# Kernel tuning notes

Measured on AMD Instinct MI355X. Metric: run time of the kernel, lower is better.

The kernel has to match this reference:

```python
import jax, jax.numpy as jnp
import numpy as np

B, T, N, M, G = 4, 16, 256, 128, 8
D, H, FFN, FD = 512, 8, 1024, 256
HD = D // H
SCALE = HD ** -0.5
EPS = 1e-5
NL = 6  # num_layers; layer 0 has no self-attn


def _ln(x, g, b):
    mu = x.mean(-1, keepdims=True)
    var = ((x - mu) ** 2).mean(-1, keepdims=True)
    return (x - mu) * jax.lax.rsqrt(var + EPS) * g + b


def setup_inputs() -> dict:
    key = jax.random.key(0)
    ks = jax.random.split(key, 16)
    w = lambda i, shape: jax.random.normal(ks[i], shape, jnp.float32) * 0.02
    return {
        'current_tokens': jax.random.normal(ks[0], (B, T, N, D), jnp.float32),
        'trajectory_tokens': jax.random.normal(ks[1], (G, M, D), jnp.float32),
        'sa_in_w': w(2, (NL - 1, 3 * D, D)), 'sa_in_b': jnp.zeros((NL - 1, 3 * D), jnp.float32),
        'sa_out_w': w(3, (NL - 1, D, D)), 'sa_out_b': jnp.zeros((NL - 1, D), jnp.float32),
        'n1_g': jnp.ones((NL - 1, D), jnp.float32), 'n1_b': jnp.zeros((NL - 1, D), jnp.float32),
        'ca_qw': w(4, (NL, D, D)), 'ca_qb': jnp.zeros((NL, D), jnp.float32),
        'ca_kw': w(5, (NL, D, D)), 'ca_kb': jnp.zeros((NL, D), jnp.float32),
        'ca_vw': w(6, (NL, D, D)), 'ca_vb': jnp.zeros((NL, D), jnp.float32),
        'ca_ow': w(7, (NL, D, D)), 'ca_ob': jnp.zeros((NL, D), jnp.float32),
        'n2_g': jnp.ones((NL, D), jnp.float32), 'n2_b': jnp.zeros((NL, D), jnp.float32),
        'f_w1': w(8, (NL, FFN, D)), 'f_b1': jnp.zeros((NL, FFN), jnp.float32),
        'f_w2': w(9, (NL, D, FFN)), 'f_b2': jnp.zeros((NL, D), jnp.float32),
        'n3_g': jnp.ones((NL, D), jnp.float32), 'n3_b': jnp.zeros((NL, D), jnp.float32),
        'out_w': w(10, (FD, D)), 'out_b': jnp.zeros((FD,), jnp.float32),
        'on_g': jnp.ones((FD,), jnp.float32), 'on_b': jnp.zeros((FD,), jnp.float32),
    }


def reference(current_tokens, trajectory_tokens, sa_in_w, sa_in_b, sa_out_w, sa_out_b,
              n1_g, n1_b, ca_qw, ca_qb, ca_kw, ca_kb, ca_vw, ca_vb, ca_ow, ca_ob,
              n2_g, n2_b, f_w1, f_b1, f_w2, f_b2, n3_g, n3_b, out_w, out_b, on_g, on_b):
    x = current_tokens
    attn_list = []
    for i in range(NL):
        if i >= 1:  # self-attention over detections within each frame
            j = i - 1
            xf = x.reshape(B * T, N, D)
            qkv = xf @ sa_in_w[j].T + sa_in_b[j]
            q, k, v = jnp.split(qkv, 3, axis=-1)
            q = q.reshape(B * T, N, H, HD)
            k = k.reshape(B * T, N, H, HD)
            v = v.reshape(B * T, N, H, HD)
            s = jnp.einsum('bnhd,bmhd->bhnm', q, k) * SCALE
            a = jax.nn.softmax(s, axis=-1)
            o = jnp.einsum('bhnm,bmhd->bnhd', a, v).reshape(B * T, N, D)
            o = o @ sa_out_w[j].T + sa_out_b[j]
            x = _ln(x + o.reshape(B, T, N, D), n1_g[j], n1_b[j])
        # cross-attention against group-averaged trajectory memory
        Q = (x @ ca_qw[i].T + ca_qb[i]).reshape(B, T, N, H, HD)
        K = (trajectory_tokens @ ca_kw[i].T + ca_kb[i]).reshape(G, M, H, HD).mean(0)  # (M,H,HD)
        V = (trajectory_tokens @ ca_vw[i].T + ca_vb[i]).reshape(G, M, H, HD).mean(0)
        s = jnp.einsum('btnhd,mhd->btnhm', Q, K) * SCALE
        # current_times=None => rel_pe_mask is zeros(T,M): no future mask; rel_pe bias is dead code in source
        a = jax.nn.softmax(s, axis=-1)  # (B,T,N,H,M)
        o = jnp.einsum('btnhm,mhd->btnhd', a, V).reshape(B, T, N, D)
        o = o @ ca_ow[i].T + ca_ob[i]
        x = _ln(x + o, n2_g[i], n2_b[i])
        # FFN
        h = jax.nn.relu(x @ f_w1[i].T + f_b1[i]) @ f_w2[i].T + f_b2[i]
        x = _ln(x + h, n3_g[i], n3_b[i])
        attn_list.append(a.mean(axis=2))  # (B,T,H,M) avg over detections
    out = _ln(x @ out_w.T + out_b, on_g, on_b)
    return out, jnp.stack(attn_list)
```

## Files before the change

kernel.cpp:

```cpp
#include <hip/hip_runtime.h>
#include <cstdint>
#include <cstddef>

#define NLl 6
#define SCALEf 0.125f
#define EPSf 1e-5f
#define Hh 8

typedef __attribute__((ext_vector_type(8))) short short8;
typedef __attribute__((ext_vector_type(4))) float float4_;
typedef __attribute__((ext_vector_type(16))) float f32x16;
typedef __attribute__((ext_vector_type(4))) int int4_;
typedef __attribute__((ext_vector_type(2))) int int2_;

__device__ inline float b2f(ushort u){ union{uint i; float f;} v; v.i = ((uint)u)<<16; return v.f; }
__device__ inline ushort f2b(float f){ union{float f; uint i;} v; v.f=f; uint r = v.i + 0x7fffu + ((v.i>>16)&1u); return (ushort)(r>>16); }
__device__ inline void unpack2(uint w, float& lo, float& hi){
  union{uint i; float f;} a,b; a.i = w<<16; b.i = w & 0xffff0000u; lo=a.f; hi=b.f;
}
__device__ inline float wred(float v){
  #pragma unroll
  for(int m=32;m>=1;m>>=1) v += __shfl_xor(v, m, 64);
  return v;
}
__device__ inline f32x16 zero16(){
  f32x16 z;
  #pragma unroll
  for(int r=0;r<16;r++) z[r]=0.f;
  return z;
}
__device__ inline int xcd_swz(int orig, int nwg){
  int q = nwg >> 3, r = nwg & 7;
  int x = orig & 7, idx = orig >> 3;
  return (x < r ? x*(q+1) : r*(q+1) + (x-r)*q) + idx;
}

struct CvtTab {
  const float* s[10];
  ushort* d[10];
  unsigned st[11];
};
__global__ __launch_bounds__(256) void cvt_all(CvtTab tab){
  unsigned g = blockIdx.x*256 + threadIdx.x;
  if (g >= tab.st[10]) return;
  int i = 0;
  #pragma unroll
  for (int k=0;k<9;k++) if (g >= tab.st[k+1]) i = k+1;
  unsigned off = g - tab.st[i];
  float4_ v = *(const float4_*)(tab.s[i] + (size_t)off*4);
  ushort o[4] = {f2b(v[0]),f2b(v[1]),f2b(v[2]),f2b(v[3])};
  *(int2_*)(tab.d[i] + (size_t)off*4) = *(const int2_*)o;
}

__global__ __launch_bounds__(256) void tmean_k(const float* __restrict__ traj, ushort* __restrict__ tm){
  int idx = blockIdx.x*256 + threadIdx.x;
  float s = 0.f;
  #pragma unroll
  for(int g=0; g<8; g++) s += traj[g*65536 + idx];
  tm[idx] = f2b(s*0.125f);
}

template<int RELU, int RESID>
__device__ __forceinline__ void gemm_core(
    const ushort* __restrict__ A, const ushort* __restrict__ W,
    const float* __restrict__ bias, const ushort* __restrict__ R,
    ushort* __restrict__ C,
    int Ndim, int K, int rowA0, int colB0,
    ushort* As, ushort* Bs)
{
  const int tid = threadIdx.x;
  const int wid = tid>>6, lane = tid&63;
  const int wr = wid>>1, wc = wid&1;
  const int l15 = lane & 15, l4 = lane >> 4;

  const ushort* gA[2]; const ushort* gB[2];
  int ldsOff[2];
  #pragma unroll
  for (int s=0;s<2;s++){
    int p = wid*128 + s*64 + lane;
    int lrow = p>>3, x = p&7;
    int logical = x ^ (lrow&7);
    int row = (logical>>2)*64 + lrow;
    int ls = logical&3;
    gA[s] = A + (size_t)(rowA0+row)*K + ls*8;
    gB[s] = W + (size_t)(colB0+row)*K + ls*8;
    ldsOff[s] = wid*1024 + s*512;
  }

  float4_ acc[4][4];
  #pragma unroll
  for(int i=0;i<4;i++)
    #pragma unroll
    for(int j=0;j<4;j++){ acc[i][j][0]=0.f; acc[i][j][1]=0.f; acc[i][j][2]=0.f; acc[i][j][3]=0.f; }

  const int NT = K >> 5;
  #pragma unroll
  for (int s=0;s<2;s++){
    __builtin_amdgcn_global_load_lds((const unsigned int*)gA[s], (unsigned int*)(As + ldsOff[s]), 16, 0, 0);
    __builtin_amdgcn_global_load_lds((const unsigned int*)gB[s], (unsigned int*)(Bs + ldsOff[s]), 16, 0, 0);
    gA[s] += 32; gB[s] += 32;
  }
  if (NT > 1){
    #pragma unroll
    for (int s=0;s<2;s++){
      __builtin_amdgcn_global_load_lds((const unsigned int*)gA[s], (unsigned int*)(As + 4096 + ldsOff[s]), 16, 0, 0);
      __builtin_amdgcn_global_load_lds((const unsigned int*)gB[s], (unsigned int*)(Bs + 4096 + ldsOff[s]), 16, 0, 0);
      gA[s] += 32; gB[s] += 32;
    }
  }

  int cur = 0;
  for (int t=0; t<NT; ++t){
    if (t+1 < NT) asm volatile("s_waitcnt vmcnt(4)" ::: "memory");
    else          asm volatile("s_waitcnt vmcnt(0)" ::: "memory");
    __builtin_amdgcn_s_barrier();
    if (t+2 < NT){
      int nb = cur+2; if (nb>=3) nb-=3;
      #pragma unroll
      for (int s=0;s<2;s++){
        __builtin_amdgcn_global_load_lds((const unsigned int*)gA[s], (unsigned int*)(As + nb*4096 + ldsOff[s]), 16, 0, 0);
        __builtin_amdgcn_global_load_lds((const unsigned int*)gB[s], (unsigned int*)(Bs + nb*4096 + ldsOff[s]), 16, 0, 0);
        gA[s] += 32; gB[s] += 32;
      }
    }
    const ushort* Apt = As + cur*4096;
    const ushort* Bpt = Bs + cur*4096;
    short8 fa[4], fb[4];
    #pragma unroll
    for(int m=0;m<4;m++){
      int lrow = m*16 + l15;
      fa[m] = *(const short8*)&Apt[lrow*64 + (((wr*4 + l4) ^ (l15&7))*8)];
    }
    #pragma unroll
    for(int n=0;n<4;n++){
      int lrow = n*16 + l15;
      fb[n] = *(const short8*)&Bpt[lrow*64 + (((wc*4 + l4) ^ (l15&7))*8)];
    }
    #pragma unroll
    for(int m=0;m<4;m++)
      #pragma unroll
      for(int n=0;n<4;n++)
        acc[m][n] = __builtin_amdgcn_mfma_f32_16x16x32_bf16(fa[m], fb[n], acc[m][n], 0,0,0);
    cur = (cur==2) ? 0 : cur+1;
  }

  #pragma unroll
  for(int m=0;m<4;m++){
    int grow = rowA0 + wr*64 + m*16 + l4*4;
    #pragma unroll
    for(int n=0;n<4;n++){
      int gcol = colB0 + wc*64 + n*16 + l15;
      float bv = bias[gcol];
      #pragma unroll
      for(int r=0;r<4;r++){
        float v = acc[m][n][r] + bv;
        if (RESID) v += b2f(R[(size_t)(grow + r)*512 + gcol]);
        if (RELU) v = fmaxf(v, 0.f);
        C[(size_t)(grow + r)*Ndim + gcol] = f2b(v);
      }
    }
  }
}

template<int RELU, int RESID>
__global__ __launch_bounds__(256, 3) void gemm_bias(
    const ushort* __restrict__ A, const ushort* __restrict__ W,
    const float* __restrict__ bias, const ushort* __restrict__ R,
    ushort* __restrict__ C, int Ndim, int K, int nbx)
{
  __shared__ ushort As[12288];
  __shared__ ushort Bs[12288];
  const int wg = xcd_swz(blockIdx.x, gridDim.x);
  const int bn = wg % nbx, bm = wg / nbx;
  gemm_core<RELU,RESID>(A, W, bias, R, C, Ndim, K, bm*128, bn*128, As, Bs);
}

__global__ __launch_bounds__(256, 3) void kv_all(
    const ushort* __restrict__ tm,
    const ushort* __restrict__ wk, const ushort* __restrict__ wv,
    const float* __restrict__ bk, const float* __restrict__ bv,
    ushort* __restrict__ KVm)
{
  __shared__ ushort As[12288];
  __shared__ ushort Bs[12288];
  const int i = blockIdx.x >> 3;
  const int r8 = blockIdx.x & 7;
  const int which = r8 >> 2, bn = r8 & 3;
  const ushort* W  = (which ? wv : wk) + (size_t)i*262144;
  const float* bias = (which ? bv : bk) + i*512;
  ushort* C = KVm + (size_t)(i*2 + which)*65536;
  gemm_core<0,0>(tm, W, bias, nullptr, C, 512, 512, 0, bn*128, As, Bs);
}

template<int NKEYS, int WRITE_ATTN, int KPF>
__global__ __launch_bounds__(256) void attn_mfma(
  const ushort* __restrict__ Qb, int qstr,
  const ushort* __restrict__ Kb, int kstr,
  const ushort* __restrict__ Vb, int vstr,
  ushort* __restrict__ Ob,
  float* __restrict__ attn_out)
{
  constexpr int NK2 = NKEYS*2;
  __shared__ __align__(16) ushort KsV[NKEYS*64 + 64*NKEYS];
  __shared__ float psum[4][NKEYS];
  const int f = blockIdx.x, h = blockIdx.y;
  const int tid = threadIdx.x, lane = tid & 63, w = tid >> 6;
  const int l31 = lane & 31, l5 = lane >> 5;
  const int swz = (lane & 7) << 4;

  ushort* Ks = KsV;
  ushort* Vt = KsV + NKEYS*64;
  const ushort* kp0 = Kb + (size_t)(KPF ? f*256 : 0)*kstr + h*64;
  const ushort* vp0 = Vb + (size_t)(KPF ? f*256 : 0)*vstr + h*64;

  for (int c = tid; c < NKEYS*8; c += 256){
    int m = c>>3, dc = c&7;
    short8 k8 = *(const short8*)(kp0 + (size_t)m*kstr + dc*8);
    short8 v8 = *(const short8*)(vp0 + (size_t)m*vstr + dc*8);
    *(short8*)((char*)Ks + m*128 + ((dc*16) ^ ((m&7)<<4))) = k8;
    #pragma unroll
    for (int j=0;j<8;j++){
      int d = dc*8 + j;
      *(ushort*)((char*)Vt + d*NK2 + ((m*2) ^ (j<<4))) = (ushort)v8[j];
    }
  }

  short8 qb[2][4];
  const int q0 = w*64;
  const ushort* qp0 = Qb + (size_t)(f*256)*qstr + h*64;
  #pragma unroll
  for (int qj=0;qj<2;qj++)
    #pragma unroll
    for (int dc=0;dc<4;dc++)
      qb[qj][dc] = *(const short8*)(qp0 + (size_t)(q0 + qj*32 + l31)*qstr + dc*16 + l5*8);
  __syncthreads();

  f32x16 O[2][2];
  O[0][0]=zero16(); O[0][1]=zero16(); O[1][0]=zero16(); O[1][1]=zero16();
  float lpart[2] = {0.f, 0.f};

  for (int t = 0; t < NKEYS/32; t++){
    const int k0 = t*32;
    short8 ka[4];
    #pragma unroll
    for (int dc=0;dc<4;dc++)
      ka[dc] = *(const short8*)((char*)Ks + (k0+l31)*128 + (((dc*32) + (l5*16)) ^ swz));
    f32x16 s0 = zero16(), s1 = zero16();
    #pragma unroll
    for (int dc=0;dc<4;dc++){
      s0 = __builtin_amdgcn_mfma_f32_32x32x16_bf16(ka[dc], qb[0][dc], s0, 0,0,0);
      s1 = __builtin_amdgcn_mfma_f32_32x32x16_bf16(ka[dc], qb[1][dc], s1, 0,0,0);
    }
    uint pw[2][8];
    #pragma unroll
    for (int qj=0;qj<2;qj++){
      const f32x16& sv = qj ? s1 : s0;
      float p[16]; float lp = 0.f;
      #pragma unroll
      for (int r=0;r<16;r++){ p[r] = __expf(sv[r]*SCALEf); lp += p[r]; }
      lpart[qj] += lp;
      #pragma unroll
      for (int k=0;k<8;k++){
        uint w_;
        asm("v_cvt_pk_bf16_f32 %0, %1, %2" : "=v"(w_) : "v"(p[2*k]), "v"(p[2*k+1]));
        pw[qj][k] = w_;
      }
    }
    short8 pa[2][2];
    #pragma unroll
    for (int qj=0;qj<2;qj++){
      #pragma unroll
      for (int mj=0;mj<2;mj++){
        uint a0 = pw[qj][mj*4+2], b0 = pw[qj][mj*4+0];
        uint a1 = pw[qj][mj*4+3], b1 = pw[qj][mj*4+1];
        asm("v_permlane32_swap_b32 %0, %1" : "+v"(a0), "+v"(b0));
        asm("v_permlane32_swap_b32 %0, %1" : "+v"(a1), "+v"(b1));
        union { uint u[4]; short8 s8; } u_;
        u_.u[0]=b0; u_.u[1]=b1; u_.u[2]=a0; u_.u[3]=a1;
        pa[qj][mj] = u_.s8;
      }
    }
    #pragma unroll
    for (int mj=0;mj<2;mj++){
      short8 vbf[2];
      #pragma unroll
      for (int dj=0;dj<2;dj++)
        vbf[dj] = *(const short8*)((char*)Vt + (dj*32+l31)*NK2 + (((k0 + mj*16 + l5*8)*2) ^ swz));
      #pragma unroll
      for (int qj=0;qj<2;qj++)
        #pragma unroll
        for (int dj=0;dj<2;dj++)
          O[qj][dj] = __builtin_amdgcn_mfma_f32_32x32x16_bf16(pa[qj][mj], vbf[dj], O[qj][dj], 0,0,0);
    }
  }

  float invl[2];
  #pragma unroll
  for (int qj=0;qj<2;qj++){
    float lt = lpart[qj] + __shfl_xor(lpart[qj], 32, 64);
    invl[qj] = 1.f / lt;
  }

  ushort* op0 = Ob + (size_t)(f*256)*512 + h*64;
  #pragma unroll
  for (int qj=0;qj<2;qj++){
    #pragma unroll
    for (int r=0;r<16;r++){
      int qr = (r&3) + 8*(r>>2) + 4*l5;
      float il = __shfl(invl[qj], (lane & 32) | qr, 64);
      #pragma unroll
      for (int dj=0;dj<2;dj++){
        float v = O[qj][dj][r] * il;
        op0[(size_t)(q0 + qj*32 + qr)*512 + dj*32 + l31] = f2b(v);
      }
    }
  }

  if (WRITE_ATTN){
    for (int t = 0; t < NKEYS/32; t++){
      const int k0 = t*32;
      short8 ka[4];
      #pragma unroll
      for (int dc=0;dc<4;dc++)
        ka[dc] = *(const short8*)((char*)Ks + (k0+l31)*128 + (((dc*32) + (l5*16)) ^ swz));
      f32x16 s0 = zero16(), s1 = zero16();
      #pragma unroll
      for (int dc=0;dc<4;dc++){
        s0 = __builtin_amdgcn_mfma_f32_32x32x16_bf16(ka[dc], qb[0][dc], s0, 0,0,0);
        s1 = __builtin_amdgcn_mfma_f32_32x32x16_bf16(ka[dc], qb[1][dc], s1, 0,0,0);
      }
      float tsum[16];
      #pragma unroll
      for (int r=0;r<16;r++){
        float v = __expf(s0[r]*SCALEf)*invl[0] + __expf(s1[r]*SCALEf)*invl[1];
        #pragma unroll
        for (int mk=1; mk<=16; mk<<=1) v += __shfl_xor(v, mk, 64);
        tsum[r] = v;
      }
      if (l31 == 0){
        #pragma unroll
        for (int r=0;r<16;r++)
          psum[w][k0 + (r&3) + 8*(r>>2) + 4*l5] = tsum[r];
      }
    }
    __syncthreads();
    for (int m = tid; m < NKEYS; m += 256){
      attn_out[f*(Hh*NKEYS) + h*NKEYS + m] =
        (psum[0][m]+psum[1][m]+psum[2][m]+psum[3][m]) * (1.0f/256.0f);
    }
  }
}

__global__ __launch_bounds__(256) void ln_post(
  const ushort* __restrict__ S,
  const float* __restrict__ g, const float* __restrict__ b,
  ushort* __restrict__ Y)
{
  const int row = blockIdx.x*4 + (threadIdx.x>>6);
  const int lane = threadIdx.x & 63;
  uint xw[4];
  *(int4_*)xw = *(const int4_*)(S + (size_t)row*512 + lane*8);
  float v[8];
  #pragma unroll
  for(int j=0;j<4;j++){ unpack2(xw[j], v[2*j], v[2*j+1]); }
  float s=0.f, sq=0.f;
  #pragma unroll
  for(int j=0;j<8;j++){ s += v[j]; sq += v[j]*v[j]; }
  s = wred(s); sq = wred(sq);
  float mu = s * (1.0f/512.0f);
  float var = sq * (1.0f/512.0f) - mu*mu;
  float rs = rsqrtf(var + EPSf);
  ushort ob[8];
  #pragma unroll
  for(int j=0;j<8;j++){
    ob[j] = f2b((v[j]-mu)*rs*g[lane*8+j] + b[lane*8+j]);
  }
  *(int4_*)(Y + (size_t)row*512 + lane*8) = *(const int4_*)ob;
}

__global__ __launch_bounds__(256) void ln_out(
  const ushort* __restrict__ A, const float* __restrict__ g,
  const float* __restrict__ b, float* __restrict__ out)
{
  const int row = blockIdx.x*4 + (threadIdx.x>>6);
  const int lane = threadIdx.x & 63;
  uint aw[2];
  *(int2_*)aw = *(const int2_*)(A + (size_t)row*256 + lane*4);
  float v[4];
  unpack2(aw[0], v[0], v[1]); unpack2(aw[1], v[2], v[3]);
  float s=0.f, sq=0.f;
  #pragma unroll
  for(int j=0;j<4;j++){ s += v[j]; sq += v[j]*v[j]; }
  s = wred(s); sq = wred(sq);
  float mu = s * (1.0f/256.0f);
  float var = sq * (1.0f/256.0f) - mu*mu;
  float rs = rsqrtf(var + EPSf);
  float4_ o;
  #pragma unroll
  for(int j=0;j<4;j++){
    o[j] = (v[j]-mu)*rs*g[lane*4+j] + b[lane*4+j];
  }
  *(float4_*)(out + (size_t)row*256 + lane*4) = o;
}

extern "C" void kernel_launch(void* const* d_in, const int* in_sizes, int n_in,
                              void* d_out, int out_size, void* d_ws, size_t ws_size,
                              hipStream_t stream) {
  const float* cur      = (const float*)d_in[0];
  const float* traj     = (const float*)d_in[1];
  const float* sa_in_w  = (const float*)d_in[2];
  const float* sa_in_b  = (const float*)d_in[3];
  const float* sa_out_w = (const float*)d_in[4];
  const float* sa_out_b = (const float*)d_in[5];
  const float* n1_g     = (const float*)d_in[6];
  const float* n1_b     = (const float*)d_in[7];
  const float* ca_qw    = (const float*)d_in[8];
  const float* ca_qb    = (const float*)d_in[9];
  const float* ca_kw    = (const float*)d_in[10];
  const float* ca_kb    = (const float*)d_in[11];
  const float* ca_vw    = (const float*)d_in[12];
  const float* ca_vb    = (const float*)d_in[13];
  const float* ca_ow    = (const float*)d_in[14];
  const float* ca_ob    = (const float*)d_in[15];
  const float* n2_g     = (const float*)d_in[16];
  const float* n2_b     = (const float*)d_in[17];
  const float* f_w1     = (const float*)d_in[18];
  const float* f_b1     = (const float*)d_in[19];
  const float* f_w2     = (const float*)d_in[20];
  const float* f_b2     = (const float*)d_in[21];
  const float* n3_g     = (const float*)d_in[22];
  const float* n3_b     = (const float*)d_in[23];
  const float* out_w    = (const float*)d_in[24];
  const float* out_b    = (const float*)d_in[25];
  const float* on_g     = (const float*)d_in[26];
  const float* on_b     = (const float*)d_in[27];

  float* out      = (float*)d_out;
  float* attn_out = out + (size_t)4*16*256*256;

  uint8_t* ws = (uint8_t*)d_ws;
  size_t off = 0;
  auto alloc = [&](size_t bytes)->uint8_t*{ uint8_t* p = ws + off; off += (bytes + 255) & ~(size_t)255; return p; };
  ushort* X   = (ushort*)alloc(16777216);
  ushort* B1  = (ushort*)alloc(50331648);
  ushort* B2  = (ushort*)alloc(16777216);
  ushort* KVm = (ushort*)alloc((size_t)6*2*65536*2);
  ushort* tm  = (ushort*)alloc(131072);
  ushort* w_sa_in  = (ushort*)alloc((size_t)5*1536*512*2);
  ushort* w_sa_out = (ushort*)alloc((size_t)5*512*512*2);
  ushort* w_ca_q   = (ushort*)alloc((size_t)6*512*512*2);
  ushort* w_ca_k   = (ushort*)alloc((size_t)6*512*512*2);
  ushort* w_ca_v   = (ushort*)alloc((size_t)6*512*512*2);
  ushort* w_ca_o   = (ushort*)alloc((size_t)6*512*512*2);
  ushort* w_f1     = (ushort*)alloc((size_t)6*1024*512*2);
  ushort* w_f2     = (ushort*)alloc((size_t)6*512*1024*2);
  ushort* w_out    = (ushort*)alloc((size_t)256*512*2);

  CvtTab tab;
  const float* srcs[10] = {cur, sa_in_w, sa_out_w, ca_qw, ca_kw, ca_vw, ca_ow, f_w1, f_w2, out_w};
  ushort* dsts[10]      = {X,   w_sa_in, w_sa_out, w_ca_q, w_ca_k, w_ca_v, w_ca_o, w_f1, w_f2, w_out};
  unsigned lens[10] = {16384u*512u, 5u*1536u*512u, 5u*512u*512u, 6u*512u*512u, 6u*512u*512u,
                       6u*512u*512u, 6u*512u*512u, 6u*1024u*512u, 6u*512u*1024u, 256u*512u};
  unsigned acc4 = 0;
  for (int i=0;i<10;i++){ tab.s[i]=srcs[i]; tab.d[i]=dsts[i]; tab.st[i]=acc4; acc4 += lens[i]/4; }
  tab.st[10] = acc4;
  cvt_all<<<(acc4+255)/256,256,0,stream>>>(tab);
  tmean_k<<<256,256,0,stream>>>(traj, tm);
  kv_all<<<48,256,0,stream>>>(tm, w_ca_k, w_ca_v, ca_kb, ca_vb, KVm);

  for (int i=0;i<NLl;i++){
    if (i>=1){
      int j = i-1;
      gemm_bias<0,0><<<12*128,256,0,stream>>>(X, w_sa_in + (size_t)j*1536*512, sa_in_b + j*1536, nullptr, B1, 1536, 512, 12);
      attn_mfma<256,0,1><<<dim3(64,8),256,0,stream>>>(B1, 1536, B1+512, 1536, B1+1024, 1536, B2, nullptr);
      gemm_bias<0,1><<<4*128,256,0,stream>>>(B2, w_sa_out + (size_t)j*262144, sa_out_b + j*512, X, B1, 512, 512, 4);
      ln_post<<<4096,256,0,stream>>>(B1, n1_g + j*512, n1_b + j*512, X);
    }
    gemm_bias<0,0><<<4*128,256,0,stream>>>(X, w_ca_q + (size_t)i*262144, ca_qb + i*512, nullptr, B2, 512, 512, 4);
    attn_mfma<128,1,0><<<dim3(64,8),256,0,stream>>>(B2, 512, KVm + (size_t)i*131072, 512, KVm + (size_t)i*131072 + 65536, 512, B1, attn_out + (size_t)i*65536);
    gemm_bias<0,1><<<4*128,256,0,stream>>>(B1, w_ca_o + (size_t)i*262144, ca_ob + i*512, X, B2, 512, 512, 4);
    ln_post<<<4096,256,0,stream>>>(B2, n2_g + i*512, n2_b + i*512, X);
    gemm_bias<1,0><<<8*128,256,0,stream>>>(X, w_f1 + (size_t)i*524288, f_b1 + i*1024, nullptr, B1, 1024, 512, 8);
    gemm_bias<0,1><<<4*128,256,0,stream>>>(B1, w_f2 + (size_t)i*524288, f_b2 + i*512, X, B2, 512, 1024, 4);
    ln_post<<<4096,256,0,stream>>>(B2, n3_g + i*512, n3_b + i*512, X);
  }
  gemm_bias<0,0><<<2*128,256,0,stream>>>(X, w_out, out_b, nullptr, B2, 256, 512, 2);
  ln_out<<<4096,256,0,stream>>>(B2, on_g, on_b, out);
}
```

Baseline: 1.316 ms.

## Load GEMM weight fragments directly to registers, drop B LDS tile

The GEMM core no longer stages the weight (B) tile through LDS. Each wave loads its B fragments straight from global memory into registers, double-buffered across an unrolled-by-two K loop, with s_setprio raised around the MFMA block. This halves LDS use per block, which could raise occupancy, and removes the B LDS writes and reads. The cost is redundant global/L2 traffic for weights shared across waves and exposed global-load latency. The attention kernel also reuses the V tile LDS region for psum, adding a barrier, to cut shared memory.

New measurement: 1.742 ms. 32.4% more time.

```diff
diff --git a/kernel.cpp b/kernel.cpp
--- a/kernel.cpp
+++ b/kernel.cpp
@@ -66,14 +66,14 @@
     const float* __restrict__ bias, const ushort* __restrict__ R,
     ushort* __restrict__ C,
     int Ndim, int K, int rowA0, int colB0,
-    ushort* As, ushort* Bs)
+    ushort* As)
 {
   const int tid = threadIdx.x;
   const int wid = tid>>6, lane = tid&63;
   const int wr = wid>>1, wc = wid&1;
   const int l15 = lane & 15, l4 = lane >> 4;
 
-  const ushort* gA[2]; const ushort* gB[2];
+  const ushort* gA[2];
   int ldsOff[2];
   #pragma unroll
   for (int s=0;s<2;s++){
@@ -83,9 +83,12 @@
     int row = (logical>>2)*64 + lrow;
     int ls = logical&3;
     gA[s] = A + (size_t)(rowA0+row)*K + ls*8;
-    gB[s] = W + (size_t)(colB0+row)*K + ls*8;
     ldsOff[s] = wid*1024 + s*512;
   }
+  const ushort* wB[4];
+  #pragma unroll
+  for (int n=0;n<4;n++)
+    wB[n] = W + (size_t)(colB0 + wc*64 + n*16 + l15)*K + l4*8;
 
   float4_ acc[4][4];
   #pragma unroll
@@ -94,54 +97,84 @@
     for(int j=0;j<4;j++){ acc[i][j][0]=0.f; acc[i][j][1]=0.f; acc[i][j][2]=0.f; acc[i][j][3]=0.f; }
 
   const int NT = K >> 5;
+  short8 fbE[4], fbO[4];
+
+  #pragma unroll
+  for (int n=0;n<4;n++) fbE[n] = *(const short8*)(wB[n]);
   #pragma unroll
   for (int s=0;s<2;s++){
     __builtin_amdgcn_global_load_lds((const unsigned int*)gA[s], (unsigned int*)(As + ldsOff[s]), 16, 0, 0);
-    __builtin_amdgcn_global_load_lds((const unsigned int*)gB[s], (unsigned int*)(Bs + ldsOff[s]), 16, 0, 0);
-    gA[s] += 32; gB[s] += 32;
-  }
-  if (NT > 1){
-    #pragma unroll
-    for (int s=0;s<2;s++){
-      __builtin_amdgcn_global_load_lds((const unsigned int*)gA[s], (unsigned int*)(As + 4096 + ldsOff[s]), 16, 0, 0);
-      __builtin_amdgcn_global_load_lds((const unsigned int*)gB[s], (unsigned int*)(Bs + 4096 + ldsOff[s]), 16, 0, 0);
-      gA[s] += 32; gB[s] += 32;
-    }
+    gA[s] += 32;
+  }
+  #pragma unroll
+  for (int s=0;s<2;s++){
+    __builtin_amdgcn_global_load_lds((const unsigned int*)gA[s], (unsigned int*)(As + 4096 + ldsOff[s]), 16, 0, 0);
+    gA[s] += 32;
   }
 
   int cur = 0;
-  for (int t=0; t<NT; ++t){
-    if (t+1 < NT) asm volatile("s_waitcnt vmcnt(4)" ::: "memory");
-    else          asm volatile("s_waitcnt vmcnt(0)" ::: "memory");
+  for (int t=0; t<NT; t+=2){
+    asm volatile("s_waitcnt vmcnt(2)" ::: "memory");
     __builtin_amdgcn_s_barrier();
-    if (t+2 < NT){
-      int nb = cur+2; if (nb>=3) nb-=3;
-      #pragma unroll
-      for (int s=0;s<2;s++){
-        __builtin_amdgcn_global_load_lds((const unsigned int*)gA[s], (unsigned int*)(As + nb*4096 + ldsOff[s]), 16, 0, 0);
-        __builtin_amdgcn_global_load_lds((const unsigned int*)gB[s], (unsigned int*)(Bs + nb*4096 + ldsOff[s]), 16, 0, 0);
-        gA[s] += 32; gB[s] += 32;
-      }
-    }
-    const ushort* Apt = As + cur*4096;
-    const ushort* Bpt = Bs + cur*4096;
-    short8 fa[4], fb[4];
-    #pragma unroll
-    for(int m=0;m<4;m++){
-      int lrow = m*16 + l15;
-      fa[m] = *(const short8*)&Apt[lrow*64 + (((wr*4 + l4) ^ (l15&7))*8)];
-    }
-    #pragma unroll
-    for(int n=0;n<4;n++){
-      int lrow = n*16 + l15;
-      fb[n] = *(const short8*)&Bpt[lrow*64 + (((wc*4 + l4) ^ (l15&7))*8)];
-    }
-    #pragma unroll
-    for(int m=0;m<4;m++)
-      #pragma unroll
-      for(int n=0;n<4;n++)
-        acc[m][n] = __builtin_amdgcn_mfma_f32_16x16x32_bf16(fa[m], fb[n], acc[m][n], 0,0,0);
-    cur = (cur==2) ? 0 : cur+1;
+    {
+      #pragma unroll
+      for (int n=0;n<4;n++) fbO[n] = *(const short8*)(wB[n] + (size_t)(t+1)*32);
+      if (t+2 < NT){
+        int nb = cur+2; if (nb>=3) nb-=3;
+        #pragma unroll
+        for (int s=0;s<2;s++){
+          __builtin_amdgcn_global_load_lds((const unsigned int*)gA[s], (unsigned int*)(As + nb*4096 + ldsOff[s]), 16, 0, 0);
+          gA[s] += 32;
+        }
+      }
+      const ushort* Apt = As + cur*4096;
+      short8 fa[4];
+      #pragma unroll
+      for(int m=0;m<4;m++){
+        int lrow = m*16 + l15;
+        fa[m] = *(const short8*)&Apt[lrow*64 + (((wr*4 + l4) ^ (l15&7))*8)];
+      }
+      __builtin_amdgcn_s_setprio(1);
+      #pragma unroll
+      for(int m=0;m<4;m++)
+        #pragma unroll
+        for(int n=0;n<4;n++)
+          acc[m][n] = __builtin_amdgcn_mfma_f32_16x16x32_bf16(fa[m], fbE[n], acc[m][n], 0,0,0);
+      __builtin_amdgcn_s_setprio(0);
+      cur = (cur==2) ? 0 : cur+1;
+    }
+    if (t+1 == NT-1) asm volatile("s_waitcnt vmcnt(0)" ::: "memory");
+    else             asm volatile("s_waitcnt vmcnt(2)" ::: "memory");
+    __builtin_amdgcn_s_barrier();
+    {
+      if (t+2 < NT){
+        #pragma unroll
+        for (int n=0;n<4;n++) fbE[n] = *(const short8*)(wB[n] + (size_t)(t+2)*32);
+      }
+      if (t+3 < NT){
+        int nb = cur+2; if (nb>=3) nb-=3;
+        #pragma unroll
+        for (int s=0;s<2;s++){
+          __builtin_amdgcn_global_load_lds((const unsigned int*)gA[s], (unsigned int*)(As + nb*4096 + ldsOff[s]), 16, 0, 0);
+          gA[s] += 32;
+        }
+      }
+      const ushort* Apt = As + cur*4096;
+      short8 fa[4];
+      #pragma unroll
+      for(int m=0;m<4;m++){
+        int lrow = m*16 + l15;
+        fa[m] = *(const short8*)&Apt[lrow*64 + (((wr*4 + l4) ^ (l15&7))*8)];
+      }
+      __builtin_amdgcn_s_setprio(1);
+      #pragma unroll
+      for(int m=0;m<4;m++)
+        #pragma unroll
+        for(int n=0;n<4;n++)
+          acc[m][n] = __builtin_amdgcn_mfma_f32_16x16x32_bf16(fa[m], fbO[n], acc[m][n], 0,0,0);
+      __builtin_amdgcn_s_setprio(0);
+      cur = (cur==2) ? 0 : cur+1;
+    }
   }
 
   #pragma unroll
@@ -169,10 +202,9 @@
     ushort* __restrict__ C, int Ndim, int K, int nbx)
 {
   __shared__ ushort As[12288];
-  __shared__ ushort Bs[12288];
   const int wg = xcd_swz(blockIdx.x, gridDim.x);
   const int bn = wg % nbx, bm = wg / nbx;
-  gemm_core<RELU,RESID>(A, W, bias, R, C, Ndim, K, bm*128, bn*128, As, Bs);
+  gemm_core<RELU,RESID>(A, W, bias, R, C, Ndim, K, bm*128, bn*128, As);
 }
 
 __global__ __launch_bounds__(256, 3) void kv_all(
@@ -182,14 +214,13 @@
     ushort* __restrict__ KVm)
 {
   __shared__ ushort As[12288];
-  __shared__ ushort Bs[12288];
   const int i = blockIdx.x >> 3;
   const int r8 = blockIdx.x & 7;
   const int which = r8 >> 2, bn = r8 & 3;
   const ushort* W  = (which ? wv : wk) + (size_t)i*262144;
   const float* bias = (which ? bv : bk) + i*512;
   ushort* C = KVm + (size_t)(i*2 + which)*65536;
-  gemm_core<0,0>(tm, W, bias, nullptr, C, 512, 512, 0, bn*128, As, Bs);
+  gemm_core<0,0>(tm, W, bias, nullptr, C, 512, 512, 0, bn*128, As);
 }
 
 template<int NKEYS, int WRITE_ATTN, int KPF>
@@ -202,7 +233,6 @@
 {
   constexpr int NK2 = NKEYS*2;
   __shared__ __align__(16) ushort KsV[NKEYS*64 + 64*NKEYS];
-  __shared__ float psum[4][NKEYS];
   const int f = blockIdx.x, h = blockIdx.y;
   const int tid = threadIdx.x, lane = tid & 63, w = tid >> 6;
   const int l31 = lane & 31, l5 = lane >> 5;
@@ -210,6 +240,7 @@
 
   ushort* Ks = KsV;
   ushort* Vt = KsV + NKEYS*64;
+  float* psum = (float*)Vt;
   const ushort* kp0 = Kb + (size_t)(KPF ? f*256 : 0)*kstr + h*64;
   const ushort* vp0 = Vb + (size_t)(KPF ? f*256 : 0)*vstr + h*64;
 
@@ -317,6 +348,7 @@
   }
 
   if (WRITE_ATTN){
+    __syncthreads();
     for (int t = 0; t < NKEYS/32; t++){
       const int k0 = t*32;
       short8 ka[4];
@@ -340,13 +372,13 @@
       if (l31 == 0){
         #pragma unroll
         for (int r=0;r<16;r++)
-          psum[w][k0 + (r&3) + 8*(r>>2) + 4*l5] = tsum[r];
+          psum[w*NKEYS + k0 + (r&3) + 8*(r>>2) + 4*l5] = tsum[r];
       }
     }
     __syncthreads();
     for (int m = tid; m < NKEYS; m += 256){
       attn_out[f*(Hh*NKEYS) + h*NKEYS + m] =
-        (psum[0][m]+psum[1][m]+psum[2][m]+psum[3][m]) * (1.0f/256.0f);
+        (psum[0*NKEYS+m]+psum[1*NKEYS+m]+psum[2*NKEYS+m]+psum[3*NKEYS+m]) * (1.0f/256.0f);
     }
   }
 }
```
